# Kernel tuning notes

Measured on AMD Instinct MI355X. Metric: run time of the kernel, lower is better.

## Reference

```python
import jax, jax.numpy as jnp
import numpy as np

# Config matching GConv(in_channels=64, out_channels=64, kernel_type=1,
#                       is_first=False, rot_1x1_in=False, stride=1, padding=1, dilation=1)
KERNEL_TYPE = 1
NUM_KERNEL = 9      # taps per sparse kernel
KERNEL_ROT = 4      # number of rotations
STEP = 8 // KERNEL_ROT
STRIDE, PAD, DIL = 1, 1, 1
CIN, COUT = 64, 64

# Ring of the 8 neighbor offsets (dy, dx) in 45-degree steps around the center.
RING = [(-1, -1), (-1, 0), (-1, 1), (0, 1), (1, 1), (1, 0), (1, -1), (0, -1)]

def tap_offsets(kernel_type, rot8):
    """Tap positions of the sparse 3x3 kernel, rotated by rot8 * 45 degrees."""
    if kernel_type == 1:      # full 3x3: center + 8 ring taps
        ring_ids = list(range(8))
    elif kernel_type == 0:    # skeleton: center + 4-cross
        ring_ids = [0, 2, 4, 6]
    else:                     # bar: center + opposite pair
        ring_ids = [0, 4]
    return [(0, 0)] + [RING[(i + rot8) % 8] for i in ring_ids]


def sparse_spatial_conv(x, w, offs):
    """x: [N, C, H, W], w: [O, C, T], offs: T tap offsets.
    Each tap contributes its own output-channel group (no tap summation):
    returns [N, T*O, Ho, Wo] with tap-major channel ordering (matches torch.cat)."""
    N, C, H, W = x.shape
    Ho = (H + 2 * PAD - (DIL * 2 + 1)) // STRIDE + 1
    Wo = (W + 2 * PAD - (DIL * 2 + 1)) // STRIDE + 1
    xp = jnp.pad(x, ((0, 0), (0, 0), (PAD, PAD), (PAD, PAD)))
    shifts = []
    for dy, dx in offs:
        sh, sw = (dy + 1) * DIL, (dx + 1) * DIL
        shifts.append(xp[:, :, sh:sh + (Ho - 1) * STRIDE + 1:STRIDE,
                             sw:sw + (Wo - 1) * STRIDE + 1:STRIDE])
    xs = jnp.stack(shifts, axis=0)               # [T, N, C, Ho, Wo]
    out = jnp.einsum('tnchw,oct->tnohw', xs, w)  # per-tap 1x1 conv at shifted pos
    Tt = out.shape[0]
    return out.transpose(1, 0, 2, 3, 4).reshape(N, Tt * w.shape[0], Ho, Wo)


def setup_inputs() -> dict:
    key = jax.random.key(0)
    k1, k2 = jax.random.split(key)
    x_tensor = jax.random.normal(k1, (8, CIN, KERNEL_ROT, 64, 64), dtype=jnp.float32)
    weight = jax.random.normal(k2, (COUT, CIN, KERNEL_ROT, NUM_KERNEL), dtype=jnp.float32) * 0.05
    return {"x_tensor": x_tensor, "weight": weight}


def reference(x_tensor, weight):
    N, Cin, R, H, W = x_tensor.shape
    # cat rotation dim into channels (rot-major): [N, R*Cin, H, W]
    x_cat = x_tensor.transpose(0, 2, 1, 3, 4).reshape(N, R * Cin, H, W)
    O = weight.shape[0]
    rot_out = []
    for rot in range(KERNEL_ROT):
        # rotated weight gather: cat weight[:, :, (idx - rot) % R, :] over idx along dim=1
        idxs = (np.arange(R) - rot) % R
        w_rot = weight[:, :, idxs, :]                    # [O, Cin, R, T]
        w_rot = w_rot.transpose(0, 2, 1, 3).reshape(O, R * Cin, NUM_KERNEL)
        offs = tap_offsets(KERNEL_TYPE, STEP * rot)
        rot_out.append(sparse_spatial_conv(x_cat, w_rot, offs))  # [N, T*O, Ho, Wo]
    return jnp.stack(rot_out, axis=2)  # [N, T*O, R, Ho, Wo]
```

## Files before the change

kernel.cpp:

```cpp
#include <hip/hip_runtime.h>
#include <stdint.h>

using short8 = __attribute__((ext_vector_type(8))) short;
using f32x4  = __attribute__((ext_vector_type(4))) float;
using u16x4  = __attribute__((ext_vector_type(4))) unsigned short;

__device__ __forceinline__ unsigned short f2bf(float f) {
    unsigned int u = __float_as_uint(f);
    unsigned int r = (u + 0x7fffu + ((u >> 16) & 1u)) >> 16;
    return (unsigned short)r;
}

__global__ __launch_bounds__(256) void k_wprep(const float* __restrict__ wgt,
                                               unsigned short* __restrict__ ball) {
    int idx = blockIdx.x * 256 + threadIdx.x;
    int k = idx & 255; int col = (idx >> 8) & 255; int j = idx >> 16;
    int rot = col >> 6, o = col & 63;
    int r = k >> 6, c = k & 63;
    int t = (j == 0) ? 0 : (1 + ((j - 1 - 2 * rot) & 7));
    float v = wgt[((o * 64 + c) * 4 + ((r - rot) & 3)) * 9 + t];
    ball[idx] = f2bf(v);
}

__global__ __launch_bounds__(512) void k_main(const float* __restrict__ x,
                                              const unsigned short* __restrict__ ball,
                                              float* __restrict__ out) {
    extern __shared__ char lds[];
    int d = blockIdx.x;
    int orig = (d & 7) * 32 + (d >> 3);
    int n = orig >> 5; int h0 = (orig & 31) * 2;
    int tid = threadIdx.x;
    unsigned short* smu = (unsigned short*)(lds + 135168);

    if (tid < 256) {
        int r4 = tid >> 6; int sp = (tid >> 5) & 1; int cc = tid & 31;
        f32x4 z = {0.f, 0.f, 0.f, 0.f};
        *(f32x4*)(lds + r4 * 33792 + (sp ? 65 * 512 : 0) + cc * 16) = z;
    }

    int klA = tid >> 2; int wq = tid & 3;
#pragma unroll 1
    for (int r4 = 0; r4 < 4; r4++) {
        int hh = h0 - 1 + r4;
        bool ok = ((unsigned)hh < 64u);
#pragma unroll 1
        for (int half = 0; half < 2; half++) {
            if (ok) {
                int k = half * 128 + klA;
                int r = k >> 6, c = k & 63;
                const float* src = x + (((size_t)(n * 64 + c) * 4 + r) * 64 + hh) * 64 + wq * 16;
#pragma unroll
                for (int i = 0; i < 4; i++) {
                    f32x4 v = *(const f32x4*)(src + i * 4);
                    u16x4 b; b[0] = f2bf(v[0]); b[1] = f2bf(v[1]);
                    b[2] = f2bf(v[2]); b[3] = f2bf(v[3]);
                    *(u16x4*)(smu + klA * 68 + wq * 16 + i * 4) = b;
                }
            } else {
                u16x4 z = {0, 0, 0, 0};
#pragma unroll
                for (int i = 0; i < 4; i++)
                    *(u16x4*)(smu + klA * 68 + wq * 16 + i * 4) = z;
            }
            __syncthreads();
            {
                int w = tid & 63; int q = tid >> 6;
                int key = (w + 1) & 7;
                char* prow = lds + (r4 * 66 + (w + 1)) * 512;
#pragma unroll
                for (int ss = 0; ss < 2; ss++) {
                    int sl = q + ss * 8;
                    int sg = half * 16 + sl;
                    short8 vv;
#pragma unroll
                    for (int e = 0; e < 8; e++) vv[e] = (short)smu[(sl * 8 + e) * 68 + w];
                    *(short8*)(prow + ((sg ^ key) << 4)) = vv;
                }
            }
            __syncthreads();
        }
    }

    int wv = tid >> 6; int l = tid & 63; int l15 = l & 15; int l4 = l >> 4;
    int rot = wv >> 1;
    const char* bb = (const char*)ball;

    for (int j = 0; j < 9; j++) {
        int dy = ((0x1A901 >> (2 * j)) & 3) - 1;
        int dx = ((0x01A91 >> (2 * j)) & 3) - 1;
        int t = (j == 0) ? 0 : (1 + ((j - 1 - 2 * rot) & 7));

        short8 Bf[2][8];
#pragma unroll
        for (int ct = 0; ct < 2; ct++) {
            int col = wv * 32 + ct * 16 + l15;
            const char* bp = bb + j * 131072 + col * 512 + l4 * 16;
#pragma unroll
            for (int ks = 0; ks < 8; ks++) Bf[ct][ks] = *(const short8*)(bp + ks * 64);
        }

#pragma unroll 1
        for (int mtp = 0; mtp < 4; mtp++) {
            short8 Af[2][8];
#pragma unroll
            for (int m2 = 0; m2 < 2; m2++) {
                int mt = mtp * 2 + m2;
                int pixel = mt * 16 + l15;
                int r4 = (pixel >> 6) + dy + 1;
                int ws = (pixel & 63) + dx + 1;
                const char* ap = lds + (r4 * 66 + ws) * 512;
                int key = ws & 7;
#pragma unroll
                for (int ks = 0; ks < 8; ks++) {
                    int s = ks * 4 + l4;
                    Af[m2][ks] = *(const short8*)(ap + ((s ^ key) << 4));
                }
            }
            f32x4 acc[2][2];
#pragma unroll
            for (int a = 0; a < 2; a++)
#pragma unroll
                for (int b2 = 0; b2 < 2; b2++) acc[a][b2] = (f32x4){0.f, 0.f, 0.f, 0.f};
            __builtin_amdgcn_s_setprio(1);
#pragma unroll
            for (int ks = 0; ks < 8; ks++)
#pragma unroll
                for (int ct = 0; ct < 2; ct++)
#pragma unroll
                    for (int m2 = 0; m2 < 2; m2++)
                        acc[ct][m2] = __builtin_amdgcn_mfma_f32_16x16x32_bf16(
                            Af[m2][ks], Bf[ct][ks], acc[ct][m2], 0, 0, 0);
            __builtin_amdgcn_s_setprio(0);
#pragma unroll
            for (int ct = 0; ct < 2; ct++) {
                int o = (wv & 1) * 32 + ct * 16 + l15;
#pragma unroll
                for (int m2 = 0; m2 < 2; m2++) {
                    int mt = mtp * 2 + m2;
                    int pb = mt * 16 + 4 * l4;
                    int h = h0 + (mt >> 2);
                    int wb = pb & 63;
                    int idx = (((n * 576 + t * 64 + o) * 4 + rot) * 64 + h) * 64 + wb;
                    *(f32x4*)(out + idx) = acc[ct][m2];
                }
            }
        }
    }
}

__global__ __launch_bounds__(256) void k_naive(const float* __restrict__ x,
                                               const float* __restrict__ wgt,
                                               float* __restrict__ out) {
    int idx = blockIdx.x * 256 + threadIdx.x;
    if (idx >= 75497472) return;
    int w = idx & 63, h = (idx >> 6) & 63, rot = (idx >> 12) & 3;
    int chn = idx >> 14; int ch = chn % 576; int n = chn / 576;
    int t = ch >> 6, o = ch & 63;
    int dy = 0, dx = 0;
    if (t > 0) {
        int ri = (t - 1 + 2 * rot) & 7;
        dy = ((27200 >> (2 * ri)) & 3) - 1;
        dx = ((1700 >> (2 * ri)) & 3) - 1;
    }
    int hh = h + dy, ww = w + dx;
    float acc = 0.f;
    if (hh >= 0 && hh < 64 && ww >= 0 && ww < 64) {
        for (int r = 0; r < 4; r++) {
            int rr = (r - rot) & 3;
            for (int c = 0; c < 64; c++)
                acc += x[(((n * 64 + c) * 4 + r) * 64 + hh) * 64 + ww] *
                       wgt[((o * 64 + c) * 4 + rr) * 9 + t];
        }
    }
    out[idx] = acc;
}

extern "C" void kernel_launch(void* const* d_in, const int* in_sizes, int n_in,
                              void* d_out, int out_size, void* d_ws, size_t ws_size,
                              hipStream_t stream) {
    const float* x = (const float*)d_in[0];
    const float* wgt = (const float*)d_in[1];
    float* out = (float*)d_out;
    const size_t NEED = (size_t)9 * 256 * 256 * 2;
    if (ws_size < NEED) {
        k_naive<<<(75497472 + 255) / 256, 256, 0, stream>>>(x, wgt, out);
        return;
    }
    unsigned short* ball = (unsigned short*)d_ws;
    k_wprep<<<2304, 256, 0, stream>>>(wgt, ball);
    k_main<<<256, 512, 152576, stream>>>(x, ball, out);
}
```

Measured before the change: 82.65 us.

## Double block to 1024 threads, splitting output rows across wave halves

New measurement: 121.0 us. +46.4%, slower.

```diff
diff --git a/kernel.cpp b/kernel.cpp
--- a/kernel.cpp
+++ b/kernel.cpp
@@ -22,9 +22,9 @@
     ball[idx] = f2bf(v);
 }
 
-__global__ __launch_bounds__(512) void k_main(const float* __restrict__ x,
-                                              const unsigned short* __restrict__ ball,
-                                              float* __restrict__ out) {
+__global__ __launch_bounds__(1024) void k_main(const float* __restrict__ x,
+                                               const unsigned short* __restrict__ ball,
+                                               float* __restrict__ out) {
     extern __shared__ char lds[];
     int d = blockIdx.x;
     int orig = (d & 7) * 32 + (d >> 3);
@@ -38,7 +38,7 @@
         *(f32x4*)(lds + r4 * 33792 + (sp ? 65 * 512 : 0) + cc * 16) = z;
     }
 
-    int klA = tid >> 2; int wq = tid & 3;
+    int klA = tid >> 3; int w8 = tid & 7;
 #pragma unroll 1
     for (int r4 = 0; r4 < 4; r4++) {
         int hh = h0 - 1 + r4;
@@ -48,101 +48,84 @@
             if (ok) {
                 int k = half * 128 + klA;
                 int r = k >> 6, c = k & 63;
-                const float* src = x + (((size_t)(n * 64 + c) * 4 + r) * 64 + hh) * 64 + wq * 16;
+                const float* src = x + (((size_t)(n * 64 + c) * 4 + r) * 64 + hh) * 64 + w8 * 8;
 #pragma unroll
-                for (int i = 0; i < 4; i++) {
+                for (int i = 0; i < 2; i++) {
                     f32x4 v = *(const f32x4*)(src + i * 4);
                     u16x4 b; b[0] = f2bf(v[0]); b[1] = f2bf(v[1]);
                     b[2] = f2bf(v[2]); b[3] = f2bf(v[3]);
-                    *(u16x4*)(smu + klA * 68 + wq * 16 + i * 4) = b;
+                    *(u16x4*)(smu + klA * 68 + w8 * 8 + i * 4) = b;
                 }
             } else {
                 u16x4 z = {0, 0, 0, 0};
 #pragma unroll
-                for (int i = 0; i < 4; i++)
-                    *(u16x4*)(smu + klA * 68 + wq * 16 + i * 4) = z;
+                for (int i = 0; i < 2; i++)
+                    *(u16x4*)(smu + klA * 68 + w8 * 8 + i * 4) = z;
             }
             __syncthreads();
             {
-                int w = tid & 63; int q = tid >> 6;
+                int w = tid & 63; int sl = tid >> 6;
                 int key = (w + 1) & 7;
                 char* prow = lds + (r4 * 66 + (w + 1)) * 512;
+                int sg = half * 16 + sl;
+                short8 vv;
 #pragma unroll
-                for (int ss = 0; ss < 2; ss++) {
-                    int sl = q + ss * 8;
-                    int sg = half * 16 + sl;
-                    short8 vv;
-#pragma unroll
-                    for (int e = 0; e < 8; e++) vv[e] = (short)smu[(sl * 8 + e) * 68 + w];
-                    *(short8*)(prow + ((sg ^ key) << 4)) = vv;
-                }
+                for (int e = 0; e < 8; e++) vv[e] = (short)smu[(sl * 8 + e) * 68 + w];
+                *(short8*)(prow + ((sg ^ key) << 4)) = vv;
             }
             __syncthreads();
         }
     }
 
     int wv = tid >> 6; int l = tid & 63; int l15 = l & 15; int l4 = l >> 4;
-    int rot = wv >> 1;
+    int m = wv >> 3;
+    int grp = wv & 7; int rot = grp >> 1;
+    int h = h0 + m;
     const char* bb = (const char*)ball;
 
     for (int j = 0; j < 9; j++) {
         int dy = ((0x1A901 >> (2 * j)) & 3) - 1;
         int dx = ((0x01A91 >> (2 * j)) & 3) - 1;
         int t = (j == 0) ? 0 : (1 + ((j - 1 - 2 * rot) & 7));
+        int r4 = m + dy + 1;
 
         short8 Bf[2][8];
 #pragma unroll
         for (int ct = 0; ct < 2; ct++) {
-            int col = wv * 32 + ct * 16 + l15;
+            int col = grp * 32 + ct * 16 + l15;
             const char* bp = bb + j * 131072 + col * 512 + l4 * 16;
 #pragma unroll
             for (int ks = 0; ks < 8; ks++) Bf[ct][ks] = *(const short8*)(bp + ks * 64);
         }
 
 #pragma unroll 1
-        for (int mtp = 0; mtp < 4; mtp++) {
-            short8 Af[2][8];
+        for (int mt = 0; mt < 4; mt++) {
+            int ws = mt * 16 + l15 + dx + 1;
+            const char* ap = lds + (r4 * 66 + ws) * 512;
+            int key = ws & 7;
+            short8 Af[8];
 #pragma unroll
-            for (int m2 = 0; m2 < 2; m2++) {
-                int mt = mtp * 2 + m2;
-                int pixel = mt * 16 + l15;
-                int r4 = (pixel >> 6) + dy + 1;
-                int ws = (pixel & 63) + dx + 1;
-                const char* ap = lds + (r4 * 66 + ws) * 512;
-                int key = ws & 7;
-#pragma unroll
-                for (int ks = 0; ks < 8; ks++) {
-                    int s = ks * 4 + l4;
-                    Af[m2][ks] = *(const short8*)(ap + ((s ^ key) << 4));
-                }
+            for (int ks = 0; ks < 8; ks++) {
+                int s = ks * 4 + l4;
+                Af[ks] = *(const short8*)(ap + ((s ^ key) << 4));
             }
-            f32x4 acc[2][2];
-#pragma unroll
-            for (int a = 0; a < 2; a++)
-#pragma unroll
-                for (int b2 = 0; b2 < 2; b2++) acc[a][b2] = (f32x4){0.f, 0.f, 0.f, 0.f};
+            f32x4 acc[2];
+            acc[0] = (f32x4){0.f, 0.f, 0.f, 0.f};
+            acc[1] = (f32x4){0.f, 0.f, 0.f, 0.f};
             __builtin_amdgcn_s_setprio(1);
 #pragma unroll
-            for (int ks = 0; ks < 8; ks++)
-#pragma unroll
-                for (int ct = 0; ct < 2; ct++)
-#pragma unroll
-                    for (int m2 = 0; m2 < 2; m2++)
-                        acc[ct][m2] = __builtin_amdgcn_mfma_f32_16x16x32_bf16(
-                            Af[m2][ks], Bf[ct][ks], acc[ct][m2], 0, 0, 0);
+            for (int ks = 0; ks < 8; ks++) {
+                acc[0] = __builtin_amdgcn_mfma_f32_16x16x32_bf16(Af[ks], Bf[0][ks], acc[0], 0, 0, 0);
+                acc[1] = __builtin_amdgcn_mfma_f32_16x16x32_bf16(Af[ks], Bf[1][ks], acc[1], 0, 0, 0);
+            }
             __builtin_amdgcn_s_setprio(0);
+            int wb = mt * 16 + 4 * l4;
 #pragma unroll
             for (int ct = 0; ct < 2; ct++) {
-                int o = (wv & 1) * 32 + ct * 16 + l15;
-#pragma unroll
-                for (int m2 = 0; m2 < 2; m2++) {
-                    int mt = mtp * 2 + m2;
-                    int pb = mt * 16 + 4 * l4;
-                    int h = h0 + (mt >> 2);
-                    int wb = pb & 63;
-                    int idx = (((n * 576 + t * 64 + o) * 4 + rot) * 64 + h) * 64 + wb;
-                    *(f32x4*)(out + idx) = acc[ct][m2];
-                }
+                int o = grp * 32 + ct * 16 + l15;
+                int oo = o & 63;
+                int idx = (((n * 576 + t * 64 + oo) * 4 + rot) * 64 + h) * 64 + wb;
+                *(f32x4*)(out + idx) = acc[ct];
             }
         }
     }
@@ -188,5 +171,5 @@
     }
     unsigned short* ball = (unsigned short*)d_ws;
     k_wprep<<<2304, 256, 0, stream>>>(wgt, ball);
-    k_main<<<256, 512, 152576, stream>>>(x, ball, out);
+    k_main<<<256, 1024, 152576, stream>>>(x, ball, out);
 }
```
